# Performance work log

Measured on AMD Instinct MI355X. Metric: run time of the kernel, lower is better.

## Reference

```python
import jax, jax.numpy as jnp
import numpy as np

DIM = 192
HEADS = 6
HEAD_DIM = DIM // HEADS
SCALE = HEAD_DIM ** -0.5


def setup_inputs() -> dict:
    key = jax.random.key(0)
    ks = jax.random.split(key, 6)
    B, H, W = 4096, 7, 7
    nW = 64
    N = H * W
    x = jax.random.normal(ks[0], (B, H, W, DIM), dtype=jnp.float32)
    mask = jax.random.normal(ks[1], (nW, N, N), dtype=jnp.float32)
    qkv_w = jax.random.normal(ks[2], (DIM, 3 * DIM), dtype=jnp.float32) * (DIM ** -0.5)
    qkv_b = jax.random.normal(ks[3], (3 * DIM,), dtype=jnp.float32) * 0.02
    proj_w = jax.random.normal(ks[4], (DIM, DIM), dtype=jnp.float32) * (DIM ** -0.5)
    proj_b = jax.random.normal(ks[5], (DIM,), dtype=jnp.float32) * 0.02
    return {"x": x, "mask": mask, "qkv_w": qkv_w, "qkv_b": qkv_b,
            "proj_w": proj_w, "proj_b": proj_b}


def reference(x, mask, qkv_w, qkv_b, proj_w, proj_b):
    B, H, W, C = x.shape
    N = H * W
    xf = x.reshape(B, N, C)
    qkv = xf @ qkv_w + qkv_b                      # [B, N, 3C]
    qkv = qkv.reshape(B, N, 3, HEADS, HEAD_DIM)
    qkv = jnp.transpose(qkv, (2, 0, 3, 1, 4))     # [3, B, h, N, d]
    q, k, v = qkv[0], qkv[1], qkv[2]
    attn = jnp.einsum('bhnd,bhmd->bhnm', q, k) * SCALE  # [B, h, N, N]
    nW = mask.shape[0]
    attn = attn.reshape(B // nW, nW, HEADS, N, N) + mask.reshape(1, nW, 1, N, N)
    attn = attn.reshape(B, HEADS, N, N)
    attn = jax.nn.softmax(attn, axis=-1)
    out = jnp.einsum('bhnm,bhmd->bnhd', attn, v).reshape(B, N, C)
    out = out @ proj_w + proj_b
    return out.reshape(B, H, W, C)
```

## Files before the change

kernel.cpp:

```cpp
#include <hip/hip_runtime.h>
#include <hip/hip_bf16.h>
#include <stdint.h>

#define NTOK 49
#define CDIM 192
#define NHEADS 6

typedef __attribute__((ext_vector_type(8))) short bf16x8;
typedef __attribute__((ext_vector_type(4))) float f32x4;

__device__ __forceinline__ short f2b(float f) {
    uint32_t u = __float_as_uint(f);
    uint32_t r = (u + 0x7fffu + ((u >> 16) & 1u)) >> 16;
    return (short)r;
}

__device__ __forceinline__ bf16x8 cvt8(const float* p) {
    f32x4 a = *(const f32x4*)p;
    f32x4 b = *(const f32x4*)(p + 4);
    union { uint32_t u[4]; bf16x8 v; } r;
    uint32_t e0 = __float_as_uint(a[0]) + 0x8000u, e1 = __float_as_uint(a[1]) + 0x8000u;
    uint32_t e2 = __float_as_uint(a[2]) + 0x8000u, e3 = __float_as_uint(a[3]) + 0x8000u;
    uint32_t e4 = __float_as_uint(b[0]) + 0x8000u, e5 = __float_as_uint(b[1]) + 0x8000u;
    uint32_t e6 = __float_as_uint(b[2]) + 0x8000u, e7 = __float_as_uint(b[3]) + 0x8000u;
    r.u[0] = __builtin_amdgcn_perm(e1, e0, 0x07060302u);
    r.u[1] = __builtin_amdgcn_perm(e3, e2, 0x07060302u);
    r.u[2] = __builtin_amdgcn_perm(e5, e4, 0x07060302u);
    r.u[3] = __builtin_amdgcn_perm(e7, e6, 0x07060302u);
    return r.v;
}

__global__ void transpose_w(const float* __restrict__ qkv_w,
                            const float* __restrict__ proj_w,
                            short* __restrict__ wt, short* __restrict__ pwt) {
    int idx = blockIdx.x * 256 + threadIdx.x;
    if (idx < CDIM * 3 * CDIM) {
        int c = idx / (3 * CDIM), j = idx % (3 * CDIM);
        wt[j * CDIM + c] = f2b(qkv_w[idx]);
    }
    if (idx < CDIM * CDIM) {
        int c = idx / CDIM, j = idx % CDIM;
        pwt[j * CDIM + c] = f2b(proj_w[idx]);
    }
}

__global__ __launch_bounds__(256, 1)
void winattn_kernel(const float* __restrict__ x, const float* __restrict__ mask,
                    const short* __restrict__ wt, const float* __restrict__ qkvb,
                    const short* __restrict__ pwt, const float* __restrict__ projb,
                    float* __restrict__ out) {
    __shared__ __align__(16) short qbuf[2][64][40];
    __shared__ __align__(16) short kbuf[2][64][40];
    __shared__ __align__(16) short vtbuf[2][32][72];
    __shared__ __align__(16) short Pbuf[4][16][72];
    __shared__ __align__(16) short Obuf[64][40];

    const int b = blockIdx.x;
    const int tid = threadIdx.x;
    const int wv = tid >> 6;
    const int lane = tid & 63;
    const int q4 = lane >> 4;
    const int l16 = lane & 15;

    const float* xg = x + (size_t)b * NTOK * CDIM;
    bf16x8 zero = {};
    bf16x8 afr[4][6];
#pragma unroll
    for (int mt = 0; mt < 4; mt++) {
        int n = mt * 16 + l16;
        const float* xr = xg + n * CDIM;
        bool valid = (n < NTOK);
#pragma unroll
        for (int ks = 0; ks < 6; ks++)
            afr[mt][ks] = valid ? cvt8(xr + ks * 32 + q4 * 8) : zero;
    }

    const float* mg = mask + (size_t)(b & 63) * NTOK * NTOK;
    float premask[4][4];
#pragma unroll
    for (int ct = 0; ct < 4; ct++)
#pragma unroll
        for (int r = 0; r < 4; r++) {
            int row = wv * 16 + q4 * 4 + r;
            int col = ct * 16 + l16;
            float mv = mg[min(row, 48) * NTOK + min(col, 48)];
            premask[ct][r] = (row < NTOK && col < NTOK) ? mv : -1e30f;
        }

    f32x4 acco[3][4];
#pragma unroll
    for (int a = 0; a < 3; a++)
#pragma unroll
        for (int m = 0; m < 4; m++) acco[a][m] = (f32x4){0.f, 0.f, 0.f, 0.f};

    const float SCALE = 0.17677669529663687f;

    for (int p = 0; p < 3; p++) {
        __syncthreads();

#pragma unroll
        for (int t = 0; t < 3; t++) {
            int i = wv * 3 + t;
            int jt;
            if (i < 4)      jt = 4 * p + i;
            else if (i < 8) jt = 12 + 4 * p + (i - 4);
            else            jt = 24 + 4 * p + (i - 8);
            int jb = jt * 16;
            const short* wrow = wt + (size_t)(jb + l16) * CDIM;
            bf16x8 bfr[6];
#pragma unroll
            for (int ks = 0; ks < 6; ks++)
                bfr[ks] = *(const bf16x8*)(wrow + ks * 32 + q4 * 8);
            f32x4 acc[4];
#pragma unroll
            for (int m = 0; m < 4; m++) acc[m] = (f32x4){0.f, 0.f, 0.f, 0.f};
#pragma unroll
            for (int ks = 0; ks < 6; ks++)
#pragma unroll
                for (int mt = 0; mt < 4; mt++)
                    acc[mt] = __builtin_amdgcn_mfma_f32_16x16x32_bf16(afr[mt][ks], bfr[ks], acc[mt], 0, 0, 0);
            float bias = qkvb[jb + l16];
            int sect = jb / CDIM;
            int jm = jb % CDIM;
            int hl = (jm / 32) - 2 * p;
            int d = (jm % 32) + l16;
#pragma unroll
            for (int mt = 0; mt < 4; mt++)
#pragma unroll
                for (int r = 0; r < 4; r++) {
                    int row = mt * 16 + q4 * 4 + r;
                    short v = f2b(acc[mt][r] + bias);
                    if (sect == 0)      qbuf[hl][row][d] = v;
                    else if (sect == 1) kbuf[hl][row][d] = v;
                    else                vtbuf[hl][d][row] = v;
                }
        }
        __syncthreads();

#pragma unroll
        for (int hl = 0; hl < 2; hl++) {
            int h = 2 * p + hl;
            f32x4 accs[4];
#pragma unroll
            for (int c = 0; c < 4; c++) accs[c] = (f32x4){0.f, 0.f, 0.f, 0.f};
            bf16x8 qa = *(const bf16x8*)&qbuf[hl][wv * 16 + l16][q4 * 8];
#pragma unroll
            for (int ct = 0; ct < 4; ct++) {
                bf16x8 kb = *(const bf16x8*)&kbuf[hl][ct * 16 + l16][q4 * 8];
                accs[ct] = __builtin_amdgcn_mfma_f32_16x16x32_bf16(qa, kb, accs[ct], 0, 0, 0);
            }
            float s[4][4], mx[4], lsum[4];
#pragma unroll
            for (int r = 0; r < 4; r++) {
                mx[r] = -3.4e38f;
#pragma unroll
                for (int ct = 0; ct < 4; ct++) {
                    s[ct][r] = accs[ct][r] * SCALE + premask[ct][r];
                    mx[r] = fmaxf(mx[r], s[ct][r]);
                }
            }
#pragma unroll
            for (int w2 = 1; w2 < 16; w2 <<= 1)
#pragma unroll
                for (int r = 0; r < 4; r++) mx[r] = fmaxf(mx[r], __shfl_xor(mx[r], w2));
#pragma unroll
            for (int r = 0; r < 4; r++) lsum[r] = 0.f;
#pragma unroll
            for (int ct = 0; ct < 4; ct++)
#pragma unroll
                for (int r = 0; r < 4; r++) {
                    float e = __expf(s[ct][r] - mx[r]);
                    s[ct][r] = e;
                    lsum[r] += e;
                }
#pragma unroll
            for (int w2 = 1; w2 < 16; w2 <<= 1)
#pragma unroll
                for (int r = 0; r < 4; r++) lsum[r] += __shfl_xor(lsum[r], w2);
#pragma unroll
            for (int ct = 0; ct < 4; ct++)
#pragma unroll
                for (int r = 0; r < 4; r++)
                    Pbuf[wv][q4 * 4 + r][ct * 16 + l16] = f2b(s[ct][r]);
            f32x4 accp[2];
            accp[0] = (f32x4){0.f, 0.f, 0.f, 0.f};
            accp[1] = (f32x4){0.f, 0.f, 0.f, 0.f};
#pragma unroll
            for (int ks = 0; ks < 2; ks++) {
                bf16x8 pa = *(const bf16x8*)&Pbuf[wv][l16][ks * 32 + q4 * 8];
#pragma unroll
                for (int jt = 0; jt < 2; jt++) {
                    bf16x8 vb = *(const bf16x8*)&vtbuf[hl][jt * 16 + l16][ks * 32 + q4 * 8];
                    accp[jt] = __builtin_amdgcn_mfma_f32_16x16x32_bf16(pa, vb, accp[jt], 0, 0, 0);
                }
            }
            __syncthreads();
            float rl[4];
#pragma unroll
            for (int r = 0; r < 4; r++) rl[r] = 1.0f / lsum[r];
#pragma unroll
            for (int jt = 0; jt < 2; jt++)
#pragma unroll
                for (int r = 0; r < 4; r++)
                    Obuf[wv * 16 + q4 * 4 + r][jt * 16 + l16] = f2b(accp[jt][r] * rl[r]);
            __syncthreads();
#pragma unroll
            for (int jtl = 0; jtl < 3; jtl++) {
                int jb = (wv * 3 + jtl) * 16;
                bf16x8 pb = *(const bf16x8*)(pwt + (size_t)(jb + l16) * CDIM + h * 32 + q4 * 8);
#pragma unroll
                for (int mt = 0; mt < 4; mt++) {
                    bf16x8 oa = *(const bf16x8*)&Obuf[mt * 16 + l16][q4 * 8];
                    acco[jtl][mt] = __builtin_amdgcn_mfma_f32_16x16x32_bf16(oa, pb, acco[jtl][mt], 0, 0, 0);
                }
            }
        }
    }

#pragma unroll
    for (int jtl = 0; jtl < 3; jtl++) {
        int jb = (wv * 3 + jtl) * 16;
        float bias = projb[jb + l16];
#pragma unroll
        for (int mt = 0; mt < 4; mt++)
#pragma unroll
            for (int r = 0; r < 4; r++) {
                int n = mt * 16 + q4 * 4 + r;
                if (n < NTOK)
                    out[((size_t)b * NTOK + n) * CDIM + jb + l16] = acco[jtl][mt][r] + bias;
            }
    }
}

extern "C" void kernel_launch(void* const* d_in, const int* in_sizes, int n_in,
                              void* d_out, int out_size, void* d_ws, size_t ws_size,
                              hipStream_t stream) {
    const float* x      = (const float*)d_in[0];
    const float* mask   = (const float*)d_in[1];
    const float* qkv_w  = (const float*)d_in[2];
    const float* qkv_b  = (const float*)d_in[3];
    const float* proj_w = (const float*)d_in[4];
    const float* proj_b = (const float*)d_in[5];
    short* wt  = (short*)d_ws;
    short* pwt = wt + CDIM * 3 * CDIM;
    float* out = (float*)d_out;
    int B = in_sizes[0] / (NTOK * CDIM);

    transpose_w<<<(CDIM * 3 * CDIM + 255) / 256, 256, 0, stream>>>(qkv_w, proj_w, wt, pwt);
    winattn_kernel<<<B, 256, 0, stream>>>(x, mask, wt, qkv_b, pwt, proj_b, out);
}
```

Measured before the change: 534.3 us.

## Split window attention into per-head kernel plus separate projection kernel

Replaces the single fused per-window kernel with one block per (window, head) that computes that head's QKV, softmax attention and output into a bf16 workspace, followed by a separate projection GEMM kernel. The goal is more parallelism and higher occupancy (launch bounds allow 4 blocks per CU versus 1) with smaller LDS use per block. In exchange, every head block re-reads and re-converts the full x tile and the mask, and the intermediate output makes an extra round trip through global memory. The old fused path is kept as a fallback when the workspace is too small.

```diff
diff --git a/kernel.cpp b/kernel.cpp
--- a/kernel.cpp
+++ b/kernel.cpp
@@ -44,6 +44,193 @@
     }
 }
 
+__global__ __launch_bounds__(256, 4)
+void attn_head_kernel(const float* __restrict__ x, const float* __restrict__ mask,
+                      const short* __restrict__ wt, const float* __restrict__ qkvb,
+                      short* __restrict__ obuf ) {
+    __shared__ __align__(16) short qbuf[64][40];
+    __shared__ __align__(16) short kbuf[64][40];
+    __shared__ __align__(16) short vtbuf[32][72];
+    __shared__ __align__(16) short Pbuf[4][16][72];
+    __shared__ __align__(16) short OSbuf[4][16][40];
+
+    const int bid = blockIdx.x;
+    const int b = bid / NHEADS;
+    const int h = bid - b * NHEADS;
+    const int tid = threadIdx.x;
+    const int wv = tid >> 6;
+    const int lane = tid & 63;
+    const int q4 = lane >> 4;
+    const int l16 = lane & 15;
+
+    const float* xg = x + (size_t)b * NTOK * CDIM;
+    bf16x8 zero = {};
+    const int n = wv * 16 + l16;
+    const bool valid = (n < NTOK);
+    const float* xr = xg + n * CDIM;
+    bf16x8 afr[6];
+#pragma unroll
+    for (int ks = 0; ks < 6; ks++)
+        afr[ks] = valid ? cvt8(xr + ks * 32 + q4 * 8) : zero;
+
+    const float* mg = mask + (size_t)(b & 63) * NTOK * NTOK;
+    float premask[4][4];
+#pragma unroll
+    for (int ct = 0; ct < 4; ct++)
+#pragma unroll
+        for (int r = 0; r < 4; r++) {
+            int row = wv * 16 + q4 * 4 + r;
+            int col = ct * 16 + l16;
+            float mv = mg[min(row, 48) * NTOK + min(col, 48)];
+            premask[ct][r] = (row < NTOK && col < NTOK) ? mv : -1e30f;
+        }
+
+#pragma unroll
+    for (int jt = 0; jt < 6; jt++) {
+        int sect = jt >> 1;
+        int jb = sect * CDIM + h * 32 + (jt & 1) * 16;
+        const short* wrow = wt + (size_t)(jb + l16) * CDIM;
+        bf16x8 bfr[6];
+#pragma unroll
+        for (int ks = 0; ks < 6; ks++)
+            bfr[ks] = *(const bf16x8*)(wrow + ks * 32 + q4 * 8);
+        f32x4 acc = (f32x4){0.f, 0.f, 0.f, 0.f};
+#pragma unroll
+        for (int ks = 0; ks < 6; ks++)
+            acc = __builtin_amdgcn_mfma_f32_16x16x32_bf16(afr[ks], bfr[ks], acc, 0, 0, 0);
+        float bias = qkvb[jb + l16];
+        int d = (jt & 1) * 16 + l16;
+#pragma unroll
+        for (int r = 0; r < 4; r++) {
+            int row = wv * 16 + q4 * 4 + r;
+            short v = f2b(acc[r] + bias);
+            if (sect == 0)      qbuf[row][d] = v;
+            else if (sect == 1) kbuf[row][d] = v;
+            else                vtbuf[d][row] = v;
+        }
+    }
+    __syncthreads();
+
+    const float SCALE = 0.17677669529663687f;
+
+    f32x4 accs[4];
+#pragma unroll
+    for (int c = 0; c < 4; c++) accs[c] = (f32x4){0.f, 0.f, 0.f, 0.f};
+    bf16x8 qa = *(const bf16x8*)&qbuf[wv * 16 + l16][q4 * 8];
+#pragma unroll
+    for (int ct = 0; ct < 4; ct++) {
+        bf16x8 kb = *(const bf16x8*)&kbuf[ct * 16 + l16][q4 * 8];
+        accs[ct] = __builtin_amdgcn_mfma_f32_16x16x32_bf16(qa, kb, accs[ct], 0, 0, 0);
+    }
+
+    float s[4][4], mx[4], lsum[4];
+#pragma unroll
+    for (int r = 0; r < 4; r++) {
+        mx[r] = -3.4e38f;
+#pragma unroll
+        for (int ct = 0; ct < 4; ct++) {
+            s[ct][r] = accs[ct][r] * SCALE + premask[ct][r];
+            mx[r] = fmaxf(mx[r], s[ct][r]);
+        }
+    }
+#pragma unroll
+    for (int w2 = 1; w2 < 16; w2 <<= 1)
+#pragma unroll
+        for (int r = 0; r < 4; r++) mx[r] = fmaxf(mx[r], __shfl_xor(mx[r], w2));
+#pragma unroll
+    for (int r = 0; r < 4; r++) lsum[r] = 0.f;
+#pragma unroll
+    for (int ct = 0; ct < 4; ct++)
+#pragma unroll
+        for (int r = 0; r < 4; r++) {
+            float e = __expf(s[ct][r] - mx[r]);
+            s[ct][r] = e;
+            lsum[r] += e;
+        }
+#pragma unroll
+    for (int w2 = 1; w2 < 16; w2 <<= 1)
+#pragma unroll
+        for (int r = 0; r < 4; r++) lsum[r] += __shfl_xor(lsum[r], w2);
+
+#pragma unroll
+    for (int ct = 0; ct < 4; ct++)
+#pragma unroll
+        for (int r = 0; r < 4; r++)
+            Pbuf[wv][q4 * 4 + r][ct * 16 + l16] = f2b(s[ct][r]);
+
+    f32x4 accp[2];
+    accp[0] = (f32x4){0.f, 0.f, 0.f, 0.f};
+    accp[1] = (f32x4){0.f, 0.f, 0.f, 0.f};
+#pragma unroll
+    for (int ks = 0; ks < 2; ks++) {
+        bf16x8 pa = *(const bf16x8*)&Pbuf[wv][l16][ks * 32 + q4 * 8];
+#pragma unroll
+        for (int jt = 0; jt < 2; jt++) {
+            bf16x8 vb = *(const bf16x8*)&vtbuf[jt * 16 + l16][ks * 32 + q4 * 8];
+            accp[jt] = __builtin_amdgcn_mfma_f32_16x16x32_bf16(pa, vb, accp[jt], 0, 0, 0);
+        }
+    }
+    float rl[4];
+#pragma unroll
+    for (int r = 0; r < 4; r++) rl[r] = 1.0f / lsum[r];
+
+#pragma unroll
+    for (int jt = 0; jt < 2; jt++)
+#pragma unroll
+        for (int r = 0; r < 4; r++)
+            OSbuf[wv][q4 * 4 + r][jt * 16 + l16] = f2b(accp[jt][r] * rl[r]);
+    bf16x8 ox = *(const bf16x8*)&OSbuf[wv][l16][q4 * 8];
+    short* op = obuf + ((size_t)(b * 64 + wv * 16 + l16)) * CDIM + h * 32 + q4 * 8;
+    *(bf16x8*)op = ox;
+}
+
+__global__ __launch_bounds__(256, 4)
+void proj_kernel(const short* __restrict__ obuf, const short* __restrict__ pwt,
+                 const float* __restrict__ projb, float* __restrict__ out) {
+    const int b = blockIdx.x;
+    const int tid = threadIdx.x;
+    const int wv = tid >> 6;
+    const int lane = tid & 63;
+    const int q4 = lane >> 4;
+    const int l16 = lane & 15;
+    const short* og = obuf + (size_t)b * 64 * CDIM;
+
+#pragma unroll
+    for (int mp = 0; mp < 2; mp++) {
+        bf16x8 afr[2][6];
+#pragma unroll
+        for (int mt = 0; mt < 2; mt++) {
+            int row = mp * 32 + mt * 16 + l16;
+#pragma unroll
+            for (int ks = 0; ks < 6; ks++)
+                afr[mt][ks] = *(const bf16x8*)(og + (size_t)row * CDIM + ks * 32 + q4 * 8);
+        }
+#pragma unroll
+        for (int jtl = 0; jtl < 3; jtl++) {
+            int jb = (wv * 3 + jtl) * 16;
+            const short* wrow = pwt + (size_t)(jb + l16) * CDIM;
+            bf16x8 bfr[6];
+#pragma unroll
+            for (int ks = 0; ks < 6; ks++)
+                bfr[ks] = *(const bf16x8*)(wrow + ks * 32 + q4 * 8);
+            float bias = projb[jb + l16];
+#pragma unroll
+            for (int mt = 0; mt < 2; mt++) {
+                f32x4 acc = (f32x4){0.f, 0.f, 0.f, 0.f};
+#pragma unroll
+                for (int ks = 0; ks < 6; ks++)
+                    acc = __builtin_amdgcn_mfma_f32_16x16x32_bf16(afr[mt][ks], bfr[ks], acc, 0, 0, 0);
+#pragma unroll
+                for (int r = 0; r < 4; r++) {
+                    int nrow = mp * 32 + mt * 16 + q4 * 4 + r;
+                    if (nrow < NTOK)
+                        out[((size_t)b * NTOK + nrow) * CDIM + jb + l16] = acc[r] + bias;
+                }
+            }
+        }
+    }
+}
+
 __global__ __launch_bounds__(256, 1)
 void winattn_kernel(const float* __restrict__ x, const float* __restrict__ mask,
                     const short* __restrict__ wt, const float* __restrict__ qkvb,
@@ -97,7 +284,6 @@
 
     for (int p = 0; p < 3; p++) {
         __syncthreads();
-
 #pragma unroll
         for (int t = 0; t < 3; t++) {
             int i = wv * 3 + t;
@@ -247,5 +433,14 @@
     int B = in_sizes[0] / (NTOK * CDIM);
 
     transpose_w<<<(CDIM * 3 * CDIM + 255) / 256, 256, 0, stream>>>(qkv_w, proj_w, wt, pwt);
-    winattn_kernel<<<B, 256, 0, stream>>>(x, mask, wt, qkv_b, pwt, proj_b, out);
-}
+
+    size_t wbytes = (size_t)(CDIM * 3 * CDIM + CDIM * CDIM) * sizeof(short);
+    size_t obytes = (size_t)B * 64 * CDIM * sizeof(short);
+    if (ws_size >= wbytes + obytes) {
+        short* obuf = pwt + CDIM * CDIM;
+        attn_head_kernel<<<B * NHEADS, 256, 0, stream>>>(x, mask, wt, qkv_b, obuf);
+        proj_kernel<<<B, 256, 0, stream>>>(obuf, pwt, proj_b, out);
+    } else {
+        winattn_kernel<<<B, 256, 0, stream>>>(x, mask, wt, qkv_b, pwt, proj_b, out);
+    }
+}
```

After: 840.4 us. 1.57x slower.

## Process both heads in parallel per wave and defer projection to one final GEMM

Applied to the files above, without the earlier changes.

Each wave now owns one head of the current pair and a 32-row half of the queries, rather than every wave looping over both heads with 16 rows. All head outputs are gathered into a full-width Obuf, and the output projection runs once at the end over K=192 instead of being accumulated per head. This drops two block barriers per head and the acco register array, and launch bounds are raised to allow two blocks per CU. The cost is more shared memory (a larger Obuf and Pbuf), which may cap occupancy, plus added register pressure from the doubled per-wave softmax state.

```diff
diff --git a/kernel.cpp b/kernel.cpp
--- a/kernel.cpp
+++ b/kernel.cpp
@@ -44,7 +44,7 @@
     }
 }
 
-__global__ __launch_bounds__(256, 1)
+__global__ __launch_bounds__(256, 2)
 void winattn_kernel(const float* __restrict__ x, const float* __restrict__ mask,
                     const short* __restrict__ wt, const float* __restrict__ qkvb,
                     const short* __restrict__ pwt, const float* __restrict__ projb,
@@ -52,8 +52,8 @@
     __shared__ __align__(16) short qbuf[2][64][40];
     __shared__ __align__(16) short kbuf[2][64][40];
     __shared__ __align__(16) short vtbuf[2][32][72];
-    __shared__ __align__(16) short Pbuf[4][16][72];
-    __shared__ __align__(16) short Obuf[64][40];
+    __shared__ __align__(16) short Pbuf[4][32][72];
+    __shared__ __align__(16) short Obuf[64][204];
 
     const int b = blockIdx.x;
     const int tid = threadIdx.x;
@@ -61,6 +61,8 @@
     const int lane = tid & 63;
     const int q4 = lane >> 4;
     const int l16 = lane & 15;
+    const int hl = wv & 1;
+    const int mh = wv >> 1;
 
     const float* xg = x + (size_t)b * NTOK * CDIM;
     bf16x8 zero = {};
@@ -76,22 +78,18 @@
     }
 
     const float* mg = mask + (size_t)(b & 63) * NTOK * NTOK;
-    float premask[4][4];
-#pragma unroll
-    for (int ct = 0; ct < 4; ct++)
-#pragma unroll
-        for (int r = 0; r < 4; r++) {
-            int row = wv * 16 + q4 * 4 + r;
-            int col = ct * 16 + l16;
-            float mv = mg[min(row, 48) * NTOK + min(col, 48)];
-            premask[ct][r] = (row < NTOK && col < NTOK) ? mv : -1e30f;
-        }
-
-    f32x4 acco[3][4];
-#pragma unroll
-    for (int a = 0; a < 3; a++)
-#pragma unroll
-        for (int m = 0; m < 4; m++) acco[a][m] = (f32x4){0.f, 0.f, 0.f, 0.f};
+    float premask[2][4][4];
+#pragma unroll
+    for (int mi = 0; mi < 2; mi++)
+#pragma unroll
+        for (int ct = 0; ct < 4; ct++)
+#pragma unroll
+            for (int r = 0; r < 4; r++) {
+                int row = mh * 32 + mi * 16 + q4 * 4 + r;
+                int col = ct * 16 + l16;
+                float mv = mg[min(row, 48) * NTOK + min(col, 48)];
+                premask[mi][ct][r] = (row < NTOK && col < NTOK) ? mv : -1e30f;
+            }
 
     const float SCALE = 0.17677669529663687f;
 
@@ -122,7 +120,7 @@
             float bias = qkvb[jb + l16];
             int sect = jb / CDIM;
             int jm = jb % CDIM;
-            int hl = (jm / 32) - 2 * p;
+            int hw = (jm / 32) - 2 * p;
             int d = (jm % 32) + l16;
 #pragma unroll
             for (int mt = 0; mt < 4; mt++)
@@ -130,105 +128,142 @@
                 for (int r = 0; r < 4; r++) {
                     int row = mt * 16 + q4 * 4 + r;
                     short v = f2b(acc[mt][r] + bias);
-                    if (sect == 0)      qbuf[hl][row][d] = v;
-                    else if (sect == 1) kbuf[hl][row][d] = v;
-                    else                vtbuf[hl][d][row] = v;
+                    if (sect == 0)      qbuf[hw][row][d] = v;
+                    else if (sect == 1) kbuf[hw][row][d] = v;
+                    else                vtbuf[hw][d][row] = v;
                 }
         }
         __syncthreads();
 
-#pragma unroll
-        for (int hl = 0; hl < 2; hl++) {
-            int h = 2 * p + hl;
-            f32x4 accs[4];
-#pragma unroll
-            for (int c = 0; c < 4; c++) accs[c] = (f32x4){0.f, 0.f, 0.f, 0.f};
-            bf16x8 qa = *(const bf16x8*)&qbuf[hl][wv * 16 + l16][q4 * 8];
+        {
+            const int h = 2 * p + hl;
+            f32x4 accs[2][4];
+#pragma unroll
+            for (int mi = 0; mi < 2; mi++)
+#pragma unroll
+                for (int c = 0; c < 4; c++) accs[mi][c] = (f32x4){0.f, 0.f, 0.f, 0.f};
+            bf16x8 qa[2];
+#pragma unroll
+            for (int mi = 0; mi < 2; mi++)
+                qa[mi] = *(const bf16x8*)&qbuf[hl][mh * 32 + mi * 16 + l16][q4 * 8];
 #pragma unroll
             for (int ct = 0; ct < 4; ct++) {
                 bf16x8 kb = *(const bf16x8*)&kbuf[hl][ct * 16 + l16][q4 * 8];
-                accs[ct] = __builtin_amdgcn_mfma_f32_16x16x32_bf16(qa, kb, accs[ct], 0, 0, 0);
-            }
-            float s[4][4], mx[4], lsum[4];
-#pragma unroll
-            for (int r = 0; r < 4; r++) {
-                mx[r] = -3.4e38f;
-#pragma unroll
-                for (int ct = 0; ct < 4; ct++) {
-                    s[ct][r] = accs[ct][r] * SCALE + premask[ct][r];
-                    mx[r] = fmaxf(mx[r], s[ct][r]);
+#pragma unroll
+                for (int mi = 0; mi < 2; mi++)
+                    accs[mi][ct] = __builtin_amdgcn_mfma_f32_16x16x32_bf16(qa[mi], kb, accs[mi][ct], 0, 0, 0);
+            }
+            float s[2][4][4], mx[2][4], lsum[2][4];
+#pragma unroll
+            for (int mi = 0; mi < 2; mi++)
+#pragma unroll
+                for (int r = 0; r < 4; r++) {
+                    mx[mi][r] = -3.4e38f;
+#pragma unroll
+                    for (int ct = 0; ct < 4; ct++) {
+                        s[mi][ct][r] = accs[mi][ct][r] * SCALE + premask[mi][ct][r];
+                        mx[mi][r] = fmaxf(mx[mi][r], s[mi][ct][r]);
+                    }
                 }
-            }
 #pragma unroll
             for (int w2 = 1; w2 < 16; w2 <<= 1)
 #pragma unroll
-                for (int r = 0; r < 4; r++) mx[r] = fmaxf(mx[r], __shfl_xor(mx[r], w2));
-#pragma unroll
-            for (int r = 0; r < 4; r++) lsum[r] = 0.f;
-#pragma unroll
-            for (int ct = 0; ct < 4; ct++)
-#pragma unroll
-                for (int r = 0; r < 4; r++) {
-                    float e = __expf(s[ct][r] - mx[r]);
-                    s[ct][r] = e;
-                    lsum[r] += e;
+                for (int mi = 0; mi < 2; mi++)
+#pragma unroll
+                    for (int r = 0; r < 4; r++) mx[mi][r] = fmaxf(mx[mi][r], __shfl_xor(mx[mi][r], w2));
+#pragma unroll
+            for (int mi = 0; mi < 2; mi++)
+#pragma unroll
+                for (int r = 0; r < 4; r++) lsum[mi][r] = 0.f;
+#pragma unroll
+            for (int mi = 0; mi < 2; mi++)
+#pragma unroll
+                for (int ct = 0; ct < 4; ct++)
+#pragma unroll
+                    for (int r = 0; r < 4; r++) {
+                        float e = __expf(s[mi][ct][r] - mx[mi][r]);
+                        s[mi][ct][r] = e;
+                        lsum[mi][r] += e;
+                    }
+#pragma unroll
+            for (int w2 = 1; w2 < 16; w2 <<= 1)
+#pragma unroll
+                for (int mi = 0; mi < 2; mi++)
+#pragma unroll
+                    for (int r = 0; r < 4; r++) lsum[mi][r] += __shfl_xor(lsum[mi][r], w2);
+#pragma unroll
+            for (int mi = 0; mi < 2; mi++)
+#pragma unroll
+                for (int ct = 0; ct < 4; ct++)
+#pragma unroll
+                    for (int r = 0; r < 4; r++)
+                        Pbuf[wv][mi * 16 + q4 * 4 + r][ct * 16 + l16] = f2b(s[mi][ct][r]);
+            f32x4 accp[2][2];
+#pragma unroll
+            for (int mi = 0; mi < 2; mi++)
+#pragma unroll
+                for (int j = 0; j < 2; j++) accp[mi][j] = (f32x4){0.f, 0.f, 0.f, 0.f};
+#pragma unroll
+            for (int ks = 0; ks < 2; ks++) {
+                bf16x8 pa[2];
+#pragma unroll
+                for (int mi = 0; mi < 2; mi++)
+                    pa[mi] = *(const bf16x8*)&Pbuf[wv][mi * 16 + l16][ks * 32 + q4 * 8];
+#pragma unroll
+                for (int jt2 = 0; jt2 < 2; jt2++) {
+                    bf16x8 vb = *(const bf16x8*)&vtbuf[hl][jt2 * 16 + l16][ks * 32 + q4 * 8];
+#pragma unroll
+                    for (int mi = 0; mi < 2; mi++)
+                        accp[mi][jt2] = __builtin_amdgcn_mfma_f32_16x16x32_bf16(pa[mi], vb, accp[mi][jt2], 0, 0, 0);
                 }
-#pragma unroll
-            for (int w2 = 1; w2 < 16; w2 <<= 1)
-#pragma unroll
-                for (int r = 0; r < 4; r++) lsum[r] += __shfl_xor(lsum[r], w2);
-#pragma unroll
-            for (int ct = 0; ct < 4; ct++)
-#pragma unroll
-                for (int r = 0; r < 4; r++)
-                    Pbuf[wv][q4 * 4 + r][ct * 16 + l16] = f2b(s[ct][r]);
-            f32x4 accp[2];
-            accp[0] = (f32x4){0.f, 0.f, 0.f, 0.f};
-            accp[1] = (f32x4){0.f, 0.f, 0.f, 0.f};
-#pragma unroll
-            for (int ks = 0; ks < 2; ks++) {
-                bf16x8 pa = *(const bf16x8*)&Pbuf[wv][l16][ks * 32 + q4 * 8];
-#pragma unroll
-                for (int jt = 0; jt < 2; jt++) {
-                    bf16x8 vb = *(const bf16x8*)&vtbuf[hl][jt * 16 + l16][ks * 32 + q4 * 8];
-                    accp[jt] = __builtin_amdgcn_mfma_f32_16x16x32_bf16(pa, vb, accp[jt], 0, 0, 0);
-                }
-            }
-            __syncthreads();
-            float rl[4];
-#pragma unroll
-            for (int r = 0; r < 4; r++) rl[r] = 1.0f / lsum[r];
-#pragma unroll
-            for (int jt = 0; jt < 2; jt++)
-#pragma unroll
-                for (int r = 0; r < 4; r++)
-                    Obuf[wv * 16 + q4 * 4 + r][jt * 16 + l16] = f2b(accp[jt][r] * rl[r]);
-            __syncthreads();
-#pragma unroll
-            for (int jtl = 0; jtl < 3; jtl++) {
-                int jb = (wv * 3 + jtl) * 16;
-                bf16x8 pb = *(const bf16x8*)(pwt + (size_t)(jb + l16) * CDIM + h * 32 + q4 * 8);
-#pragma unroll
-                for (int mt = 0; mt < 4; mt++) {
-                    bf16x8 oa = *(const bf16x8*)&Obuf[mt * 16 + l16][q4 * 8];
-                    acco[jtl][mt] = __builtin_amdgcn_mfma_f32_16x16x32_bf16(oa, pb, acco[jtl][mt], 0, 0, 0);
-                }
+            }
+#pragma unroll
+            for (int mi = 0; mi < 2; mi++) {
+                float rl[4];
+#pragma unroll
+                for (int r = 0; r < 4; r++) rl[r] = 1.0f / lsum[mi][r];
+#pragma unroll
+                for (int jt2 = 0; jt2 < 2; jt2++)
+#pragma unroll
+                    for (int r = 0; r < 4; r++)
+                        Obuf[mh * 32 + mi * 16 + q4 * 4 + r][h * 32 + jt2 * 16 + l16] =
+                            f2b(accp[mi][jt2][r] * rl[r]);
             }
         }
     }
 
+    __syncthreads();
+
+    bf16x8 pb[3][6];
 #pragma unroll
     for (int jtl = 0; jtl < 3; jtl++) {
         int jb = (wv * 3 + jtl) * 16;
-        float bias = projb[jb + l16];
-#pragma unroll
-        for (int mt = 0; mt < 4; mt++)
+        const short* wrow = pwt + (size_t)(jb + l16) * CDIM;
+#pragma unroll
+        for (int ks = 0; ks < 6; ks++)
+            pb[jtl][ks] = *(const bf16x8*)(wrow + ks * 32 + q4 * 8);
+    }
+#pragma unroll
+    for (int mt = 0; mt < 4; mt++) {
+        bf16x8 oafr[6];
+#pragma unroll
+        for (int ks = 0; ks < 6; ks++)
+            oafr[ks] = *(const bf16x8*)&Obuf[mt * 16 + l16][ks * 32 + q4 * 8];
+#pragma unroll
+        for (int jtl = 0; jtl < 3; jtl++) {
+            int jb = (wv * 3 + jtl) * 16;
+            f32x4 acc = (f32x4){0.f, 0.f, 0.f, 0.f};
+#pragma unroll
+            for (int ks = 0; ks < 6; ks++)
+                acc = __builtin_amdgcn_mfma_f32_16x16x32_bf16(oafr[ks], pb[jtl][ks], acc, 0, 0, 0);
+            float bias = projb[jb + l16];
 #pragma unroll
             for (int r = 0; r < 4; r++) {
                 int n = mt * 16 + q4 * 4 + r;
                 if (n < NTOK)
-                    out[((size_t)b * NTOK + n) * CDIM + jb + l16] = acco[jtl][mt][r] + bias;
-            }
+                    out[((size_t)b * NTOK + n) * CDIM + jb + l16] = acc[r] + bias;
+            }
+        }
     }
 }
 
```

Result: faster. 519.8 us (-2.7%).

## Split heads across waves, batch projection per head pair, raise occupancy

Applied to the files above, without the earlier changes.

Waves are repartitioned so each wave owns one head of the current pair and half of the token rows, instead of all four waves walking the two heads one after the other. Both heads' outputs now go into a wider Obuf, and the output projection runs once per pair with K=64, which drops two block-wide barriers per head. The mask is reloaded from global memory inside the loop rather than held in registers, and LDS row padding is reduced. Together with launch bounds raised to 3 blocks per CU, this aims to cut barrier stalls and fit more resident blocks. The trade-offs are extra mask loads and 16-byte LDS vector reads on rows whose strides are no longer 16-byte aligned.

```diff
diff --git a/kernel.cpp b/kernel.cpp
--- a/kernel.cpp
+++ b/kernel.cpp
@@ -44,16 +44,16 @@
     }
 }
 
-__global__ __launch_bounds__(256, 1)
+__global__ __launch_bounds__(256, 3)
 void winattn_kernel(const float* __restrict__ x, const float* __restrict__ mask,
                     const short* __restrict__ wt, const float* __restrict__ qkvb,
                     const short* __restrict__ pwt, const float* __restrict__ projb,
                     float* __restrict__ out) {
-    __shared__ __align__(16) short qbuf[2][64][40];
-    __shared__ __align__(16) short kbuf[2][64][40];
-    __shared__ __align__(16) short vtbuf[2][32][72];
-    __shared__ __align__(16) short Pbuf[4][16][72];
-    __shared__ __align__(16) short Obuf[64][40];
+    __shared__ __align__(16) short qbuf[2][64][36];
+    __shared__ __align__(16) short kbuf[2][64][36];
+    __shared__ __align__(16) short vtbuf[2][32][68];
+    __shared__ __align__(16) short Pbuf[4][16][68];
+    __shared__ __align__(16) short Obuf[64][66];
 
     const int b = blockIdx.x;
     const int tid = threadIdx.x;
@@ -61,31 +61,24 @@
     const int lane = tid & 63;
     const int q4 = lane >> 4;
     const int l16 = lane & 15;
+    const int hl = wv & 1;
+    const int mh = wv >> 1;
+    const int jh = wv & 1;
 
     const float* xg = x + (size_t)b * NTOK * CDIM;
     bf16x8 zero = {};
-    bf16x8 afr[4][6];
-#pragma unroll
-    for (int mt = 0; mt < 4; mt++) {
-        int n = mt * 16 + l16;
+    bf16x8 afr[2][6];
+#pragma unroll
+    for (int m = 0; m < 2; m++) {
+        int n = (mh * 2 + m) * 16 + l16;
         const float* xr = xg + n * CDIM;
         bool valid = (n < NTOK);
 #pragma unroll
         for (int ks = 0; ks < 6; ks++)
-            afr[mt][ks] = valid ? cvt8(xr + ks * 32 + q4 * 8) : zero;
+            afr[m][ks] = valid ? cvt8(xr + ks * 32 + q4 * 8) : zero;
     }
 
     const float* mg = mask + (size_t)(b & 63) * NTOK * NTOK;
-    float premask[4][4];
-#pragma unroll
-    for (int ct = 0; ct < 4; ct++)
-#pragma unroll
-        for (int r = 0; r < 4; r++) {
-            int row = wv * 16 + q4 * 4 + r;
-            int col = ct * 16 + l16;
-            float mv = mg[min(row, 48) * NTOK + min(col, 48)];
-            premask[ct][r] = (row < NTOK && col < NTOK) ? mv : -1e30f;
-        }
 
     f32x4 acco[3][4];
 #pragma unroll
@@ -99,8 +92,8 @@
         __syncthreads();
 
 #pragma unroll
-        for (int t = 0; t < 3; t++) {
-            int i = wv * 3 + t;
+        for (int t = 0; t < 6; t++) {
+            int i = jh * 6 + t;
             int jt;
             if (i < 4)      jt = 4 * p + i;
             else if (i < 8) jt = 12 + 4 * p + (i - 4);
@@ -111,39 +104,48 @@
 #pragma unroll
             for (int ks = 0; ks < 6; ks++)
                 bfr[ks] = *(const bf16x8*)(wrow + ks * 32 + q4 * 8);
-            f32x4 acc[4];
-#pragma unroll
-            for (int m = 0; m < 4; m++) acc[m] = (f32x4){0.f, 0.f, 0.f, 0.f};
+            f32x4 acc[2];
+            acc[0] = (f32x4){0.f, 0.f, 0.f, 0.f};
+            acc[1] = (f32x4){0.f, 0.f, 0.f, 0.f};
 #pragma unroll
             for (int ks = 0; ks < 6; ks++)
 #pragma unroll
-                for (int mt = 0; mt < 4; mt++)
-                    acc[mt] = __builtin_amdgcn_mfma_f32_16x16x32_bf16(afr[mt][ks], bfr[ks], acc[mt], 0, 0, 0);
+                for (int m = 0; m < 2; m++)
+                    acc[m] = __builtin_amdgcn_mfma_f32_16x16x32_bf16(afr[m][ks], bfr[ks], acc[m], 0, 0, 0);
             float bias = qkvb[jb + l16];
             int sect = jb / CDIM;
             int jm = jb % CDIM;
-            int hl = (jm / 32) - 2 * p;
+            int hw = (jm / 32) - 2 * p;
             int d = (jm % 32) + l16;
 #pragma unroll
-            for (int mt = 0; mt < 4; mt++)
+            for (int m = 0; m < 2; m++)
 #pragma unroll
                 for (int r = 0; r < 4; r++) {
-                    int row = mt * 16 + q4 * 4 + r;
-                    short v = f2b(acc[mt][r] + bias);
-                    if (sect == 0)      qbuf[hl][row][d] = v;
-                    else if (sect == 1) kbuf[hl][row][d] = v;
-                    else                vtbuf[hl][d][row] = v;
+                    int row = (mh * 2 + m) * 16 + q4 * 4 + r;
+                    short v = f2b(acc[m][r] + bias);
+                    if (sect == 0)      qbuf[hw][row][d] = v;
+                    else if (sect == 1) kbuf[hw][row][d] = v;
+                    else                vtbuf[hw][d][row] = v;
                 }
         }
         __syncthreads();
 
 #pragma unroll
-        for (int hl = 0; hl < 2; hl++) {
-            int h = 2 * p + hl;
+        for (int mi = 0; mi < 2; mi++) {
+            float premask[4][4];
+#pragma unroll
+            for (int ct = 0; ct < 4; ct++)
+#pragma unroll
+                for (int r = 0; r < 4; r++) {
+                    int row = mh * 32 + mi * 16 + q4 * 4 + r;
+                    int col = ct * 16 + l16;
+                    float mv = mg[min(row, 48) * NTOK + min(col, 48)];
+                    premask[ct][r] = (row < NTOK && col < NTOK) ? mv : -1e30f;
+                }
+            bf16x8 qa = *(const bf16x8*)&qbuf[hl][mh * 32 + mi * 16 + l16][q4 * 8];
             f32x4 accs[4];
 #pragma unroll
             for (int c = 0; c < 4; c++) accs[c] = (f32x4){0.f, 0.f, 0.f, 0.f};
-            bf16x8 qa = *(const bf16x8*)&qbuf[hl][wv * 16 + l16][q4 * 8];
 #pragma unroll
             for (int ct = 0; ct < 4; ct++) {
                 bf16x8 kb = *(const bf16x8*)&kbuf[hl][ct * 16 + l16][q4 * 8];
@@ -189,29 +191,36 @@
             for (int ks = 0; ks < 2; ks++) {
                 bf16x8 pa = *(const bf16x8*)&Pbuf[wv][l16][ks * 32 + q4 * 8];
 #pragma unroll
-                for (int jt = 0; jt < 2; jt++) {
-                    bf16x8 vb = *(const bf16x8*)&vtbuf[hl][jt * 16 + l16][ks * 32 + q4 * 8];
-                    accp[jt] = __builtin_amdgcn_mfma_f32_16x16x32_bf16(pa, vb, accp[jt], 0, 0, 0);
-                }
-            }
-            __syncthreads();
+                for (int jt2 = 0; jt2 < 2; jt2++) {
+                    bf16x8 vb = *(const bf16x8*)&vtbuf[hl][jt2 * 16 + l16][ks * 32 + q4 * 8];
+                    accp[jt2] = __builtin_amdgcn_mfma_f32_16x16x32_bf16(pa, vb, accp[jt2], 0, 0, 0);
+                }
+            }
             float rl[4];
 #pragma unroll
             for (int r = 0; r < 4; r++) rl[r] = 1.0f / lsum[r];
 #pragma unroll
-            for (int jt = 0; jt < 2; jt++)
+            for (int jt2 = 0; jt2 < 2; jt2++)
 #pragma unroll
                 for (int r = 0; r < 4; r++)
-                    Obuf[wv * 16 + q4 * 4 + r][jt * 16 + l16] = f2b(accp[jt][r] * rl[r]);
-            __syncthreads();
-#pragma unroll
-            for (int jtl = 0; jtl < 3; jtl++) {
-                int jb = (wv * 3 + jtl) * 16;
-                bf16x8 pb = *(const bf16x8*)(pwt + (size_t)(jb + l16) * CDIM + h * 32 + q4 * 8);
-#pragma unroll
-                for (int mt = 0; mt < 4; mt++) {
-                    bf16x8 oa = *(const bf16x8*)&Obuf[mt * 16 + l16][q4 * 8];
-                    acco[jtl][mt] = __builtin_amdgcn_mfma_f32_16x16x32_bf16(oa, pb, acco[jtl][mt], 0, 0, 0);
+                    Obuf[mh * 32 + mi * 16 + q4 * 4 + r][hl * 32 + jt2 * 16 + l16] =
+                        f2b(accp[jt2][r] * rl[r]);
+        }
+        __syncthreads();
+
+#pragma unroll
+        for (int jtl = 0; jtl < 3; jtl++) {
+            int jb = (wv * 3 + jtl) * 16;
+            const short* wrow = pwt + (size_t)(jb + l16) * CDIM + p * 64;
+            bf16x8 pb[2];
+            pb[0] = *(const bf16x8*)(wrow + q4 * 8);
+            pb[1] = *(const bf16x8*)(wrow + 32 + q4 * 8);
+#pragma unroll
+            for (int mt = 0; mt < 4; mt++) {
+#pragma unroll
+                for (int ks = 0; ks < 2; ks++) {
+                    bf16x8 oa = *(const bf16x8*)&Obuf[mt * 16 + l16][ks * 32 + q4 * 8];
+                    acco[jtl][mt] = __builtin_amdgcn_mfma_f32_16x16x32_bf16(oa, pb[ks], acco[jtl][mt], 0, 0, 0);
                 }
             }
         }
```

Result: slower. 644.6 us (+20.6%).
